# Optimization experiments

Hardware: AMD Instinct MI355X
Metric: run time of the kernel (lower is better)

Reference implementation:

```python
import jax, jax.numpy as jnp
import numpy as np

N = 50000      # nodes
E = 500000     # edges
MUL = 32       # multiplicity of 0e and 1o in node irreps
NUM_NEIGHBORS = 10.0
MIX = 0.15
INV3 = 1.0 / np.sqrt(3.0)  # sqrt(2*l3+1)*wigner_3j(1,1,0) = delta_ij/sqrt(3)


def setup_inputs() -> dict:
    key = jax.random.key(0)
    ks = jax.random.split(key, 16)
    f32 = jnp.float32
    node_input = jax.random.normal(ks[0], (N, 128), dtype=f32)  # 32x0e (32) + 32x1o (96)
    # edge_attr = spherical harmonics lmax=1, component normalization: Y0=1, |Y1|=sqrt(3)
    y1 = jax.random.normal(ks[1], (E, 3), dtype=f32)
    y1 = jnp.sqrt(3.0) * y1 / jnp.linalg.norm(y1, axis=1, keepdims=True)
    edge_attr = jnp.concatenate([jnp.ones((E, 1), f32), y1], axis=1)  # [E,4]
    edge_scalars = jax.random.uniform(ks[2], (E, 8), dtype=f32)       # radial embedding
    edge_src = jax.random.randint(ks[3], (E,), 0, N)
    edge_dst = jax.random.randint(ks[4], (E,), 0, N)
    rn = lambda k, s: jax.random.normal(k, s, dtype=f32)
    return {
        "node_input": node_input, "edge_attr": edge_attr, "edge_scalars": edge_scalars,
        "W1_s": rn(ks[5], (MUL, 2 * MUL)),  # first Linear, 0e block: 32 -> 64 (=feat 32 + self 32)
        "W1_v": rn(ks[6], (MUL, 2 * MUL)),  # first Linear, 1o block
        "M0": rn(ks[7], (8, 32)), "M1": rn(ks[8], (32, 32)),  # weight MLP (fc_neurons=[32,32])
        "Wtp0": rn(ks[9], (32, MUL)),   # path 0e x 0e -> 0e
        "Wtp1": rn(ks[10], (32, MUL)),  # path 0e x 1o -> 1o
        "Wtp2": rn(ks[11], (32, MUL)),  # path 1o x 0e -> 1o
        "Wtp3": rn(ks[12], (32, MUL)),  # path 1o x 1o -> 0e
        "W2_s": rn(ks[13], (2 * MUL, MUL)),  # final Linear, 0e: 64 -> 32
        "W2_v": rn(ks[14], (2 * MUL, MUL)),  # final Linear, 1o: 64 -> 32
        "edge_src": edge_src, "edge_dst": edge_dst,
    }


def _forward(node_input, edge_attr, edge_scalars, W1_s, W1_v, M0, M1,
             Wtp0, Wtp1, Wtp2, Wtp3, W2_s, W2_v, edge_src, edge_dst):
    n = node_input.shape[0]
    s = node_input[:, :MUL]                       # [N,32]  0e
    v = node_input[:, MUL:].reshape(n, MUL, 3)    # [N,32,3] 1o
    # Linear(node_input.irreps + irreps_out): per-irrep mixing, fan-in normalized
    s_all = (s @ W1_s) / jnp.sqrt(jnp.float32(MUL))                    # [N,64]
    v_all = jnp.einsum('nuk,uw->nwk', v, W1_v) / jnp.sqrt(jnp.float32(MUL))  # [N,64,3]
    feat_s, self_s = s_all[:, :MUL], s_all[:, MUL:]
    feat_v, self_v = v_all[:, :MUL], v_all[:, MUL:]

    # gather by edge source
    es = feat_s[edge_src]   # [E,32]
    ev = feat_v[edge_src]   # [E,32,3]
    y0 = edge_attr[:, 0]    # [E]
    y1 = edge_attr[:, 1:4]  # [E,3]

    # MLP on edge scalars -> per-edge, per-path 'uvu' weights (fan-in normalized)
    h = jax.nn.gelu(edge_scalars @ M0 / jnp.sqrt(jnp.float32(8)))
    h = jax.nn.gelu(h @ M1 / jnp.sqrt(jnp.float32(32)))                # [E,32]
    inv_sqrt_h = 1.0 / jnp.sqrt(jnp.float32(32))
    w0 = (h @ Wtp0) * inv_sqrt_h  # [E,32]
    w1 = (h @ Wtp1) * inv_sqrt_h
    w2 = (h @ Wtp2) * inv_sqrt_h
    w3 = (h @ Wtp3) * inv_sqrt_h

    # per-edge CG tensor product (4 'uvu' instructions)
    out0a = w0 * es * y0[:, None]                                    # 0e x 0e -> 0e
    out0b = w3 * jnp.einsum('euk,ek->eu', ev, y1) * INV3             # 1o x 1o -> 0e
    out1a = w1[:, :, None] * es[:, :, None] * y1[:, None, :]        # 0e x 1o -> 1o
    out1b = w2[:, :, None] * ev * y0[:, None, None]                 # 1o x 0e -> 1o
    out0 = jnp.concatenate([out0a, out0b], axis=1)                  # [E,64]  64x0e
    out1 = jnp.concatenate([out1a, out1b], axis=1)                  # [E,64,3] 64x1o

    # scatter-add to destination nodes, normalize by sqrt(num_neighbors)
    inv_deg = 1.0 / jnp.sqrt(jnp.float32(NUM_NEIGHBORS))
    ns = jax.ops.segment_sum(out0, edge_dst, num_segments=n) * inv_deg              # [N,64]
    nv = jax.ops.segment_sum(out1.reshape(-1, 2 * MUL * 3), edge_dst,
                             num_segments=n).reshape(n, 2 * MUL, 3) * inv_deg       # [N,64,3]

    # final per-irrep Linear to output irreps 32x0e + 32x1o
    conv_s = (ns @ W2_s) / jnp.sqrt(jnp.float32(2 * MUL))
    conv_v = jnp.einsum('nuk,uw->nwk', nv, W2_v) / jnp.sqrt(jnp.float32(2 * MUL))

    a = jnp.sqrt(jnp.float32(1.0 - MIX))
    b = jnp.sqrt(jnp.float32(MIX))
    out_s = a * self_s + b * conv_s                                  # [N,32]
    out_v = (a * self_v + b * conv_v).reshape(n, MUL * 3)            # [N,96]
    return jnp.concatenate([out_s, out_v], axis=1)                   # [N,128]


def reference(node_input, edge_attr, edge_scalars, W1_s, W1_v, M0, M1,
              Wtp0, Wtp1, Wtp2, Wtp3, W2_s, W2_v, edge_src, edge_dst):
    return _forward(node_input, edge_attr, edge_scalars, W1_s, W1_v, M0, M1,
                    Wtp0, Wtp1, Wtp2, Wtp3, W2_s, W2_v, edge_src, edge_dst)
```

## Files before the change

### kernel.cpp

```cpp
#include <hip/hip_runtime.h>
#include <math.h>

#define N_NODES 50000
#define N_EDGES 500000
#define NPB 8
#define GROUPS 8

__device__ __forceinline__ float gelu_fast(float x) {
    const float k0 = 0.7978845608028654f;
    const float k1 = 0.044715f;
    float z2 = 2.f * k0 * (x + k1 * x * x * x);
    float ez = __expf(z2);
    float th = 1.f - 2.f * __builtin_amdgcn_rcpf(ez + 1.f);
    return 0.5f * x * (1.f + th);
}

__device__ __forceinline__ unsigned short f2bf(float x) {
    unsigned int u = __float_as_uint(x);
    unsigned int r = (u + 0x7FFFu + ((u >> 16) & 1u)) >> 16;
    return (unsigned short)r;
}
__device__ __forceinline__ unsigned int pack2bf(float a, float b) {
    return (unsigned int)f2bf(a) | ((unsigned int)f2bf(b) << 16);
}
__device__ __forceinline__ float bf_lo(unsigned int w) {
    return __uint_as_float(w << 16);
}
__device__ __forceinline__ float bf_hi(unsigned int w) {
    return __uint_as_float(w & 0xffff0000u);
}

__device__ __forceinline__ void lds_add(float* p, float v) {
    unsigned int off = (unsigned int)(size_t)p;
    asm volatile("ds_add_f32 %0, %1" :: "v"(off), "v"(v) : "memory");
}

__global__ void node_pre(const float* __restrict__ node_input,
                         const float* __restrict__ W1_s,
                         const float* __restrict__ W1_v,
                         float* __restrict__ feat,
                         float* __restrict__ out) {
    __shared__ float lWs[32 * 64];
    __shared__ float lWv[32 * 64];
    for (int i = threadIdx.x; i < 2048; i += blockDim.x) {
        lWs[i] = W1_s[i];
        lWv[i] = W1_v[i];
    }
    __syncthreads();
    int n = blockIdx.x * blockDim.x + threadIdx.x;
    if (n >= N_NODES) return;
    const float inv_sqrt_mul = 0.17677669529663687f;
    const float a_mix = 0.9219544457292887f;

    float s[32];
#pragma unroll
    for (int u = 0; u < 32; ++u) s[u] = node_input[n * 128 + u];
#pragma unroll 4
    for (int w = 0; w < 64; ++w) {
        float acc = 0.f;
#pragma unroll
        for (int u = 0; u < 32; ++u) acc += s[u] * lWs[u * 64 + w];
        acc *= inv_sqrt_mul;
        if (w < 32) feat[(size_t)n * 128 + w * 4 + 0] = acc;
        else        out[n * 128 + (w - 32)] = a_mix * acc;
    }
#pragma unroll
    for (int k = 0; k < 3; ++k) {
        float vk[32];
#pragma unroll
        for (int u = 0; u < 32; ++u) vk[u] = node_input[n * 128 + 32 + u * 3 + k];
#pragma unroll 4
        for (int w = 0; w < 64; ++w) {
            float acc = 0.f;
#pragma unroll
            for (int u = 0; u < 32; ++u) acc += vk[u] * lWv[u * 64 + w];
            acc *= inv_sqrt_mul;
            if (w < 32) feat[(size_t)n * 128 + w * 4 + 1 + k] = acc;
            else        out[n * 128 + 32 + (w - 32) * 3 + k] = a_mix * acc;
        }
    }
}

__global__ void hist_kernel(const int* __restrict__ edge_dst, int* __restrict__ counts) {
    int e = blockIdx.x * blockDim.x + threadIdx.x;
    if (e < N_EDGES) atomicAdd(&counts[edge_dst[e]], 1);
}

__global__ void scan_kernel(const int* __restrict__ counts,
                            int* __restrict__ offsets,
                            int* __restrict__ cursor) {
    const int T = 1024;
    __shared__ int partial[T];
    int t = threadIdx.x;
    const int chunk = (N_NODES + T - 1) / T;
    int start = t * chunk;
    int end = start + chunk; if (end > N_NODES) end = N_NODES;
    if (start > N_NODES) start = N_NODES;
    int sum = 0;
    for (int i = start; i < end; ++i) sum += counts[i];
    partial[t] = sum;
    __syncthreads();
    for (int off = 1; off < T; off <<= 1) {
        int other = (t >= off) ? partial[t - off] : 0;
        __syncthreads();
        partial[t] += other;
        __syncthreads();
    }
    int run = (t == 0) ? 0 : partial[t - 1];
    for (int i = start; i < end; ++i) {
        offsets[i] = run;
        cursor[i] = run;
        run += counts[i];
    }
    if (t == T - 1) offsets[N_NODES] = run;
}

__global__ void scatter_kernel(const int* __restrict__ edge_src,
                               const int* __restrict__ edge_dst,
                               const float* __restrict__ edge_attr,
                               int* __restrict__ cursor,
                               float4* __restrict__ ySorted,
                               int2* __restrict__ srcdst,
                               int* __restrict__ epos) {
    int e = blockIdx.x * blockDim.x + threadIdx.x;
    if (e >= N_EDGES) return;
    int d = edge_dst[e];
    int pos = atomicAdd(&cursor[d], 1);
    ySorted[pos] = *(const float4*)(edge_attr + (size_t)e * 4);
    srcdst[pos] = make_int2(edge_src[e], d);
    epos[e] = pos;
}

__global__ void __launch_bounds__(256)
h_kernel(const float* __restrict__ edge_scalars,
         const int* __restrict__ epos,
         const float* __restrict__ M0,
         const float* __restrict__ M1,
         uint4* __restrict__ hSorted) {
    const int e = blockIdx.x * blockDim.x + threadIdx.x;
    if (e >= N_EDGES) return;

    const float inv_sqrt8  = 0.35355339059327373f;
    const float inv_sqrt32 = 0.17677669529663687f;

    const float4 s0 = *(const float4*)(edge_scalars + (size_t)e * 8);
    const float4 s1 = *(const float4*)(edge_scalars + (size_t)e * 8 + 4);
    const int pos = epos[e];

    float t[32];
#pragma unroll
    for (int u = 0; u < 32; ++u) {
        float acc = s0.x * M0[0 * 32 + u] + s0.y * M0[1 * 32 + u]
                  + s0.z * M0[2 * 32 + u] + s0.w * M0[3 * 32 + u]
                  + s1.x * M0[4 * 32 + u] + s1.y * M0[5 * 32 + u]
                  + s1.z * M0[6 * 32 + u] + s1.w * M0[7 * 32 + u];
        t[u] = gelu_fast(acc * inv_sqrt8);
    }
    float h[32];
#pragma unroll
    for (int u = 0; u < 32; ++u) {
        float acc = 0.f;
#pragma unroll
        for (int m = 0; m < 32; ++m) acc += t[m] * M1[m * 32 + u];
        h[u] = gelu_fast(acc * inv_sqrt32);
    }

    uint4* dst = hSorted + (size_t)pos * 4;
#pragma unroll
    for (int c = 0; c < 4; ++c) {
        uint4 pk;
        pk.x = pack2bf(h[c * 8 + 0], h[c * 8 + 1]);
        pk.y = pack2bf(h[c * 8 + 2], h[c * 8 + 3]);
        pk.z = pack2bf(h[c * 8 + 4], h[c * 8 + 5]);
        pk.w = pack2bf(h[c * 8 + 6], h[c * 8 + 7]);
        dst[c] = pk;
    }
}

__global__ void __launch_bounds__(256)
conv_kernel(const uint4* __restrict__ hSorted,
            const float4* __restrict__ ySorted,
            const int2* __restrict__ srcdst,
            const int* __restrict__ offsets,
            const float* __restrict__ Wtp0,
            const float* __restrict__ Wtp1,
            const float* __restrict__ Wtp2,
            const float* __restrict__ Wtp3,
            const float* __restrict__ W2_s,
            const float* __restrict__ W2_v,
            const float* __restrict__ feat,
            float* __restrict__ out) {
    __shared__ float sacc[NPB * 256];
    for (int i = threadIdx.x; i < NPB * 256; i += blockDim.x) sacc[i] = 0.f;

    const int lane = threadIdx.x & 31;
    const int g = threadIdx.x >> 5;

    const float inv_sqrt32 = 0.17677669529663687f;
    unsigned int wA[32], wB[32];
#pragma unroll
    for (int j = 0; j < 32; ++j) {
        wA[j] = pack2bf(Wtp0[j * 32 + lane] * inv_sqrt32,
                        Wtp1[j * 32 + lane] * inv_sqrt32);
        wB[j] = pack2bf(Wtp2[j * 32 + lane] * inv_sqrt32,
                        Wtp3[j * 32 + lane] * inv_sqrt32);
    }
    __syncthreads();

    const int n0 = blockIdx.x * NPB;
    const int eb = offsets[n0];
    const int ee = offsets[n0 + NPB];
    const float INV3 = 0.5773502691896258f;
    const float4* feat4 = (const float4*)feat;

    const int total = ee - eb;
    const int per = (total + GROUPS - 1) / GROUPS;
    const int es = eb + g * per;
    int et = es + per; if (et > ee) et = ee;

    float r0 = 0.f, r1 = 0.f, r2 = 0.f, r3 = 0.f;
    float r4 = 0.f, r5 = 0.f, r6 = 0.f, r7 = 0.f;
    int cur = -1;

    if (es < et) {
        const int last = et - 1;
        int2 sd = srcdst[es];
        float4 yq = ySorted[es];
        uint4 h0 = hSorted[(size_t)es * 4 + 0];
        uint4 h1 = hSorted[(size_t)es * 4 + 1];
        uint4 h2 = hSorted[(size_t)es * 4 + 2];
        uint4 h3 = hSorted[(size_t)es * 4 + 3];
        float4 f = feat4[(size_t)sd.x * 32 + lane];
        int e1 = es + 1 <= last ? es + 1 : last;
        int2 sdN = srcdst[e1];

        for (int e = es; e < et; ++e) {
            const int ep1 = e + 1 <= last ? e + 1 : last;
            const int ep2 = e + 2 <= last ? e + 2 : last;
            float4 yqN = ySorted[ep1];
            uint4 h0N = hSorted[(size_t)ep1 * 4 + 0];
            uint4 h1N = hSorted[(size_t)ep1 * 4 + 1];
            uint4 h2N = hSorted[(size_t)ep1 * 4 + 2];
            uint4 h3N = hSorted[(size_t)ep1 * 4 + 3];
            float4 fN = feat4[(size_t)sdN.x * 32 + lane];
            int2 sdNN = srcdst[ep2];

            if (sd.y != cur) {
                if (cur >= 0) {
                    float* ap = sacc + (cur - n0) * 256;
                    lds_add(ap + lane, r0);
                    lds_add(ap + 32 + lane, r1);
                    lds_add(ap + 64 + lane * 3 + 0, r2);
                    lds_add(ap + 64 + lane * 3 + 1, r3);
                    lds_add(ap + 64 + lane * 3 + 2, r4);
                    lds_add(ap + 160 + lane * 3 + 0, r5);
                    lds_add(ap + 160 + lane * 3 + 1, r6);
                    lds_add(ap + 160 + lane * 3 + 2, r7);
                }
                cur = sd.y;
                r0 = r1 = r2 = r3 = r4 = r5 = r6 = r7 = 0.f;
            }

            float w0 = 0.f, w1 = 0.f, w2 = 0.f, w3 = 0.f;
            const unsigned int hw[16] = {h0.x, h0.y, h0.z, h0.w,
                                         h1.x, h1.y, h1.z, h1.w,
                                         h2.x, h2.y, h2.z, h2.w,
                                         h3.x, h3.y, h3.z, h3.w};
#pragma unroll
            for (int k = 0; k < 16; ++k) {
                const float hlo = bf_lo(hw[k]);
                const float hhi = bf_hi(hw[k]);
                const unsigned int a0 = wA[2 * k],     b0 = wB[2 * k];
                const unsigned int a1 = wA[2 * k + 1], b1 = wB[2 * k + 1];
                w0 += hlo * bf_lo(a0); w1 += hlo * bf_hi(a0);
                w2 += hlo * bf_lo(b0); w3 += hlo * bf_hi(b0);
                w0 += hhi * bf_lo(a1); w1 += hhi * bf_hi(a1);
                w2 += hhi * bf_lo(b1); w3 += hhi * bf_hi(b1);
            }

            const float dvy = f.y * yq.y + f.z * yq.z + f.w * yq.w;
            const float w1es = w1 * f.x;
            const float w2y0 = w2 * yq.x;

            r0 += w0 * f.x * yq.x;
            r1 += w3 * dvy * INV3;
            r2 += w1es * yq.y;
            r3 += w1es * yq.z;
            r4 += w1es * yq.w;
            r5 += w2y0 * f.y;
            r6 += w2y0 * f.z;
            r7 += w2y0 * f.w;

            sd = sdN; sdN = sdNN;
            yq = yqN; h0 = h0N; h1 = h1N; h2 = h2N; h3 = h3N; f = fN;
        }
        if (cur >= 0) {
            float* ap = sacc + (cur - n0) * 256;
            lds_add(ap + lane, r0);
            lds_add(ap + 32 + lane, r1);
            lds_add(ap + 64 + lane * 3 + 0, r2);
            lds_add(ap + 64 + lane * 3 + 1, r3);
            lds_add(ap + 64 + lane * 3 + 2, r4);
            lds_add(ap + 160 + lane * 3 + 0, r5);
            lds_add(ap + 160 + lane * 3 + 1, r6);
            lds_add(ap + 160 + lane * 3 + 2, r7);
        }
    }
    asm volatile("s_waitcnt lgkmcnt(0)" ::: "memory");
    __syncthreads();

    const float scale = 0.31622776601683794f * 0.125f * 0.3872983346207417f;
    {
        const int li = g;
        const float* ap = sacc + li * 256;
        float cs = 0.f, cv0 = 0.f, cv1 = 0.f, cv2 = 0.f;
#pragma unroll 8
        for (int j = 0; j < 64; ++j) {
            const float as = ap[j];
            cs += as * __ldg(&W2_s[j * 32 + lane]);
            const float wv = __ldg(&W2_v[j * 32 + lane]);
            cv0 += ap[64 + 3 * j + 0] * wv;
            cv1 += ap[64 + 3 * j + 1] * wv;
            cv2 += ap[64 + 3 * j + 2] * wv;
        }
        float* o = out + (size_t)(n0 + li) * 128;
        o[lane]              += scale * cs;
        o[32 + lane * 3 + 0] += scale * cv0;
        o[32 + lane * 3 + 1] += scale * cv1;
        o[32 + lane * 3 + 2] += scale * cv2;
    }
}

extern "C" void kernel_launch(void* const* d_in, const int* in_sizes, int n_in,
                              void* d_out, int out_size, void* d_ws, size_t ws_size,
                              hipStream_t stream) {
    const float* node_input   = (const float*)d_in[0];
    const float* edge_attr    = (const float*)d_in[1];
    const float* edge_scalars = (const float*)d_in[2];
    const float* W1_s = (const float*)d_in[3];
    const float* W1_v = (const float*)d_in[4];
    const float* M0   = (const float*)d_in[5];
    const float* M1   = (const float*)d_in[6];
    const float* Wtp0 = (const float*)d_in[7];
    const float* Wtp1 = (const float*)d_in[8];
    const float* Wtp2 = (const float*)d_in[9];
    const float* Wtp3 = (const float*)d_in[10];
    const float* W2_s = (const float*)d_in[11];
    const float* W2_v = (const float*)d_in[12];
    const int* edge_src = (const int*)d_in[13];
    const int* edge_dst = (const int*)d_in[14];
    float* out = (float*)d_out;
    float* ws  = (float*)d_ws;

    float*  feat    = ws;
    float4* ySorted = (float4*)(feat + (size_t)N_NODES * 128);
    uint4*  hSorted = (uint4*)(ySorted + N_EDGES);
    int2*   srcdst  = (int2*)(hSorted + (size_t)N_EDGES * 4);
    int*    epos    = (int*)(srcdst + N_EDGES);
    int*    counts  = epos + N_EDGES;
    int*    offsets = counts + N_NODES;
    int*    cursor  = offsets + N_NODES + 1;

    hipMemsetAsync(counts, 0, N_NODES * sizeof(int), stream);

    node_pre<<<(N_NODES + 255) / 256, 256, 0, stream>>>(node_input, W1_s, W1_v,
                                                        feat, out);

    hist_kernel<<<(N_EDGES + 255) / 256, 256, 0, stream>>>(edge_dst, counts);
    scan_kernel<<<1, 1024, 0, stream>>>(counts, offsets, cursor);
    scatter_kernel<<<(N_EDGES + 255) / 256, 256, 0, stream>>>(edge_src, edge_dst,
                                                              edge_attr, cursor,
                                                              ySorted, srcdst, epos);

    h_kernel<<<(N_EDGES + 255) / 256, 256, 0, stream>>>(edge_scalars, epos,
                                                        M0, M1, hSorted);

    conv_kernel<<<N_NODES / NPB, 256, 0, stream>>>(hSorted, ySorted, srcdst, offsets,
                                                   Wtp0, Wtp1, Wtp2, Wtp3,
                                                   W2_s, W2_v, feat, out);
}
```

Baseline: 572.3 us.

## Move tensor-product weights to LDS and drop software prefetch to raise occupancy

The packed bf16 tensor-product weights move out of 64 per-thread registers into a shared LDS table that each edge iteration reads with uint4 loads. The one-edge-ahead software prefetch is removed and launch bounds request 6 blocks per CU, cutting register pressure so more waves can hide gather latency. The cost is 16 extra LDS reads per edge and no explicit prefetch overlap, so latency hiding now depends on occupancy.

```diff
diff --git a/kernel.cpp b/kernel.cpp
--- a/kernel.cpp
+++ b/kernel.cpp
@@ -177,7 +177,7 @@
     }
 }
 
-__global__ void __launch_bounds__(256)
+__global__ void __launch_bounds__(256, 6)
 conv_kernel(const uint4* __restrict__ hSorted,
             const float4* __restrict__ ySorted,
             const int2* __restrict__ srcdst,
@@ -191,22 +191,25 @@
             const float* __restrict__ feat,
             float* __restrict__ out) {
     __shared__ float sacc[NPB * 256];
+    __shared__ uint4 lW[16 * 32];
+
     for (int i = threadIdx.x; i < NPB * 256; i += blockDim.x) sacc[i] = 0.f;
+
+    const float inv_sqrt32 = 0.17677669529663687f;
+    for (int idx = threadIdx.x; idx < 512; idx += blockDim.x) {
+        const int k = idx >> 5, ln = idx & 31;
+        const int j0 = 2 * k, j1 = 2 * k + 1;
+        uint4 w;
+        w.x = pack2bf(Wtp0[j0 * 32 + ln] * inv_sqrt32, Wtp1[j0 * 32 + ln] * inv_sqrt32);
+        w.y = pack2bf(Wtp2[j0 * 32 + ln] * inv_sqrt32, Wtp3[j0 * 32 + ln] * inv_sqrt32);
+        w.z = pack2bf(Wtp0[j1 * 32 + ln] * inv_sqrt32, Wtp1[j1 * 32 + ln] * inv_sqrt32);
+        w.w = pack2bf(Wtp2[j1 * 32 + ln] * inv_sqrt32, Wtp3[j1 * 32 + ln] * inv_sqrt32);
+        lW[idx] = w;
+    }
+    __syncthreads();
 
     const int lane = threadIdx.x & 31;
     const int g = threadIdx.x >> 5;
-
-    const float inv_sqrt32 = 0.17677669529663687f;
-    unsigned int wA[32], wB[32];
-#pragma unroll
-    for (int j = 0; j < 32; ++j) {
-        wA[j] = pack2bf(Wtp0[j * 32 + lane] * inv_sqrt32,
-                        Wtp1[j * 32 + lane] * inv_sqrt32);
-        wB[j] = pack2bf(Wtp2[j * 32 + lane] * inv_sqrt32,
-                        Wtp3[j * 32 + lane] * inv_sqrt32);
-    }
-    __syncthreads();
-
     const int n0 = blockIdx.x * NPB;
     const int eb = offsets[n0];
     const int ee = offsets[n0 + NPB];
@@ -222,89 +225,70 @@
     float r4 = 0.f, r5 = 0.f, r6 = 0.f, r7 = 0.f;
     int cur = -1;
 
-    if (es < et) {
-        const int last = et - 1;
-        int2 sd = srcdst[es];
-        float4 yq = ySorted[es];
-        uint4 h0 = hSorted[(size_t)es * 4 + 0];
-        uint4 h1 = hSorted[(size_t)es * 4 + 1];
-        uint4 h2 = hSorted[(size_t)es * 4 + 2];
-        uint4 h3 = hSorted[(size_t)es * 4 + 3];
-        float4 f = feat4[(size_t)sd.x * 32 + lane];
-        int e1 = es + 1 <= last ? es + 1 : last;
-        int2 sdN = srcdst[e1];
-
-        for (int e = es; e < et; ++e) {
-            const int ep1 = e + 1 <= last ? e + 1 : last;
-            const int ep2 = e + 2 <= last ? e + 2 : last;
-            float4 yqN = ySorted[ep1];
-            uint4 h0N = hSorted[(size_t)ep1 * 4 + 0];
-            uint4 h1N = hSorted[(size_t)ep1 * 4 + 1];
-            uint4 h2N = hSorted[(size_t)ep1 * 4 + 2];
-            uint4 h3N = hSorted[(size_t)ep1 * 4 + 3];
-            float4 fN = feat4[(size_t)sdN.x * 32 + lane];
-            int2 sdNN = srcdst[ep2];
-
-            if (sd.y != cur) {
-                if (cur >= 0) {
-                    float* ap = sacc + (cur - n0) * 256;
-                    lds_add(ap + lane, r0);
-                    lds_add(ap + 32 + lane, r1);
-                    lds_add(ap + 64 + lane * 3 + 0, r2);
-                    lds_add(ap + 64 + lane * 3 + 1, r3);
-                    lds_add(ap + 64 + lane * 3 + 2, r4);
-                    lds_add(ap + 160 + lane * 3 + 0, r5);
-                    lds_add(ap + 160 + lane * 3 + 1, r6);
-                    lds_add(ap + 160 + lane * 3 + 2, r7);
-                }
-                cur = sd.y;
-                r0 = r1 = r2 = r3 = r4 = r5 = r6 = r7 = 0.f;
+    for (int e = es; e < et; ++e) {
+        const int2 sd = srcdst[e];
+        const float4 yq = ySorted[e];
+        const uint4 h0 = hSorted[(size_t)e * 4 + 0];
+        const uint4 h1 = hSorted[(size_t)e * 4 + 1];
+        const uint4 h2 = hSorted[(size_t)e * 4 + 2];
+        const uint4 h3 = hSorted[(size_t)e * 4 + 3];
+        const float4 f = feat4[(size_t)sd.x * 32 + lane];
+
+        if (sd.y != cur) {
+            if (cur >= 0) {
+                float* ap = sacc + (cur - n0) * 256;
+                lds_add(ap + lane, r0);
+                lds_add(ap + 32 + lane, r1);
+                lds_add(ap + 64 + lane * 3 + 0, r2);
+                lds_add(ap + 64 + lane * 3 + 1, r3);
+                lds_add(ap + 64 + lane * 3 + 2, r4);
+                lds_add(ap + 160 + lane * 3 + 0, r5);
+                lds_add(ap + 160 + lane * 3 + 1, r6);
+                lds_add(ap + 160 + lane * 3 + 2, r7);
             }
-
-            float w0 = 0.f, w1 = 0.f, w2 = 0.f, w3 = 0.f;
-            const unsigned int hw[16] = {h0.x, h0.y, h0.z, h0.w,
-                                         h1.x, h1.y, h1.z, h1.w,
-                                         h2.x, h2.y, h2.z, h2.w,
-                                         h3.x, h3.y, h3.z, h3.w};
-#pragma unroll
-            for (int k = 0; k < 16; ++k) {
-                const float hlo = bf_lo(hw[k]);
-                const float hhi = bf_hi(hw[k]);
-                const unsigned int a0 = wA[2 * k],     b0 = wB[2 * k];
-                const unsigned int a1 = wA[2 * k + 1], b1 = wB[2 * k + 1];
-                w0 += hlo * bf_lo(a0); w1 += hlo * bf_hi(a0);
-                w2 += hlo * bf_lo(b0); w3 += hlo * bf_hi(b0);
-                w0 += hhi * bf_lo(a1); w1 += hhi * bf_hi(a1);
-                w2 += hhi * bf_lo(b1); w3 += hhi * bf_hi(b1);
-            }
-
-            const float dvy = f.y * yq.y + f.z * yq.z + f.w * yq.w;
-            const float w1es = w1 * f.x;
-            const float w2y0 = w2 * yq.x;
-
-            r0 += w0 * f.x * yq.x;
-            r1 += w3 * dvy * INV3;
-            r2 += w1es * yq.y;
-            r3 += w1es * yq.z;
-            r4 += w1es * yq.w;
-            r5 += w2y0 * f.y;
-            r6 += w2y0 * f.z;
-            r7 += w2y0 * f.w;
-
-            sd = sdN; sdN = sdNN;
-            yq = yqN; h0 = h0N; h1 = h1N; h2 = h2N; h3 = h3N; f = fN;
+            cur = sd.y;
+            r0 = r1 = r2 = r3 = r4 = r5 = r6 = r7 = 0.f;
         }
-        if (cur >= 0) {
-            float* ap = sacc + (cur - n0) * 256;
-            lds_add(ap + lane, r0);
-            lds_add(ap + 32 + lane, r1);
-            lds_add(ap + 64 + lane * 3 + 0, r2);
-            lds_add(ap + 64 + lane * 3 + 1, r3);
-            lds_add(ap + 64 + lane * 3 + 2, r4);
-            lds_add(ap + 160 + lane * 3 + 0, r5);
-            lds_add(ap + 160 + lane * 3 + 1, r6);
-            lds_add(ap + 160 + lane * 3 + 2, r7);
+
+        float w0 = 0.f, w1 = 0.f, w2 = 0.f, w3 = 0.f;
+        const unsigned int hw[16] = {h0.x, h0.y, h0.z, h0.w,
+                                     h1.x, h1.y, h1.z, h1.w,
+                                     h2.x, h2.y, h2.z, h2.w,
+                                     h3.x, h3.y, h3.z, h3.w};
+#pragma unroll
+        for (int k = 0; k < 16; ++k) {
+            const uint4 wk = lW[k * 32 + lane];
+            const float hlo = bf_lo(hw[k]);
+            const float hhi = bf_hi(hw[k]);
+            w0 += hlo * bf_lo(wk.x); w1 += hlo * bf_hi(wk.x);
+            w2 += hlo * bf_lo(wk.y); w3 += hlo * bf_hi(wk.y);
+            w0 += hhi * bf_lo(wk.z); w1 += hhi * bf_hi(wk.z);
+            w2 += hhi * bf_lo(wk.w); w3 += hhi * bf_hi(wk.w);
         }
+
+        const float dvy = f.y * yq.y + f.z * yq.z + f.w * yq.w;
+        const float w1es = w1 * f.x;
+        const float w2y0 = w2 * yq.x;
+
+        r0 += w0 * f.x * yq.x;
+        r1 += w3 * dvy * INV3;
+        r2 += w1es * yq.y;
+        r3 += w1es * yq.z;
+        r4 += w1es * yq.w;
+        r5 += w2y0 * f.y;
+        r6 += w2y0 * f.z;
+        r7 += w2y0 * f.w;
+    }
+    if (cur >= 0) {
+        float* ap = sacc + (cur - n0) * 256;
+        lds_add(ap + lane, r0);
+        lds_add(ap + 32 + lane, r1);
+        lds_add(ap + 64 + lane * 3 + 0, r2);
+        lds_add(ap + 64 + lane * 3 + 1, r3);
+        lds_add(ap + 64 + lane * 3 + 2, r4);
+        lds_add(ap + 160 + lane * 3 + 0, r5);
+        lds_add(ap + 160 + lane * 3 + 1, r6);
+        lds_add(ap + 160 + lane * 3 + 2, r7);
     }
     asm volatile("s_waitcnt lgkmcnt(0)" ::: "memory");
     __syncthreads();
```

Result: faster. 556.0 us (-2.8%).
